# Optimization experiments

Measured on AMD Instinct MI355X. Metric: run time of the kernel, lower is better.

The kernel has to match this reference:

```python
import jax, jax.numpy as jnp
import numpy as np

THRESHOLD = 0.5
NEG_POS_RATIO = 3
ALPHA = 1.0


def xywh2xyxy(b):
    return jnp.concatenate([b[:, :2], b[:, :2] + b[:, 2:]], axis=1)


def cxcy2xyxy(b):
    return jnp.concatenate([b[:, :2] - b[:, 2:] / 2, b[:, :2] + b[:, 2:] / 2], axis=1)


def xyxy2cxcy(b):
    return jnp.concatenate([(b[:, :2] + b[:, 2:]) / 2, b[:, 2:] - b[:, :2]], axis=1)


def jaccard(a, b):
    # a: [n,4], b: [m,4] in xyxy -> IoU [n,m]
    lt = jnp.maximum(a[:, None, :2], b[None, :, :2])
    rb = jnp.minimum(a[:, None, 2:], b[None, :, 2:])
    wh = jnp.clip(rb - lt, 0.0)
    inter = wh[..., 0] * wh[..., 1]
    area_a = (a[:, 2] - a[:, 0]) * (a[:, 3] - a[:, 1])
    area_b = (b[:, 2] - b[:, 0]) * (b[:, 3] - b[:, 1])
    return inter / (area_a[:, None] + area_b[None, :] - inter)


def encode(cxcy, priors_cxcy):
    # cxcy_to_gcxgcy: offsets scaled by /10 variance, log sizes scaled by *5
    return jnp.concatenate([
        (cxcy[:, :2] - priors_cxcy[:, :2]) / (priors_cxcy[:, 2:] / 10.0),
        jnp.log(jnp.abs(cxcy[:, 2:] / priors_cxcy[:, 2:])) * 5.0,
    ], axis=1)


def _match_one(boxes_xywh, labels_i, priors_xy, priors_cxcy):
    n_obj = boxes_xywh.shape[0]
    b_xyxy = xywh2xyxy(boxes_xywh)                      # [n_obj,4]
    ov = jaccard(b_xyxy, priors_xy)                     # [n_obj, P]
    ovl_p = ov.max(axis=0)                              # [P]
    obj_p = ov.argmax(axis=0)                           # [P]
    prior_for_obj = ov.argmax(axis=1)                   # [n_obj]
    # force each object to own its best prior
    obj_p = obj_p.at[prior_for_obj].set(jnp.arange(n_obj))
    ovl_p = ovl_p.at[prior_for_obj].set(1.0)
    lab = labels_i[obj_p]                               # [P]
    lab = jnp.where(ovl_p < THRESHOLD, 0, lab)
    ignore = (ovl_p > 0.4) & (ovl_p < 0.5)
    true_locs = encode(xyxy2cxcy(b_xyxy[obj_p]), priors_cxcy)  # [P,4]
    return lab, ignore, true_locs


def _smooth_l1(x):
    ax = jnp.abs(x)
    return jnp.where(ax < 1.0, 0.5 * ax * ax, ax - 0.5)


def multibox_loss(predicted_locs, predicted_scores, boxes, labels, priors_cxcy):
    priors_xy = cxcy2xyxy(priors_cxcy)
    true_classes, ignored, true_locs = jax.vmap(
        _match_one, in_axes=(0, 0, None, None))(boxes, labels, priors_xy, priors_cxcy)
    pos = (true_classes > 0) & (~ignored)               # [B,P]
    n_pos = pos.sum(axis=1)                             # [B]
    n_pos_total = n_pos.sum()

    # localization loss: SmoothL1 mean over positive-prior elements
    loc_elem = _smooth_l1(predicted_locs - true_locs)   # [B,P,4]
    loc_loss = (loc_elem * pos[..., None]).sum() / (n_pos_total.astype(jnp.float32) * 4.0)

    # per-prior cross entropy
    logp = jax.nn.log_softmax(predicted_scores, axis=-1)           # [B,P,C]
    ce = -jnp.take_along_axis(logp, true_classes[..., None], axis=-1)[..., 0]  # [B,P]

    conf_pos_sum = (ce * pos).sum()
    ce_neg = jnp.where(pos | ignored, 0.0, ce)
    ce_neg_sorted = -jnp.sort(-ce_neg, axis=1)          # descending per row
    ranks = jnp.arange(ce.shape[1])[None, :]
    hard = ranks < (NEG_POS_RATIO * n_pos)[:, None]
    conf_loss = (jnp.where(hard, ce_neg_sorted, 0.0).sum() + conf_pos_sum) / n_pos_total.astype(jnp.float32)

    total = conf_loss + ALPHA * loc_loss
    return total, conf_loss, loc_loss


def setup_inputs() -> dict:
    key = jax.random.key(0)
    k1, k2, k3, k4, k5, k6 = jax.random.split(key, 6)
    B, P, C, NOBJ = 64, 8732, 91, 16
    predicted_locs = jax.random.normal(k1, (B, P, 4), dtype=jnp.float32)
    predicted_scores = jax.random.normal(k2, (B, P, C), dtype=jnp.float32)
    xy = jax.random.uniform(k3, (B, NOBJ, 2)) * 0.6
    wh = jax.random.uniform(k4, (B, NOBJ, 2)) * 0.35 + 0.05
    boxes = jnp.concatenate([xy, wh], axis=-1).astype(jnp.float32)  # xywh
    labels = jax.random.randint(k5, (B, NOBJ), 1, C)
    pxy = jax.random.uniform(k6, (P, 2))
    pwh = jax.random.uniform(jax.random.fold_in(k6, 1), (P, 2)) * 0.45 + 0.05
    priors_cxcy = jnp.concatenate([pxy, pwh], axis=-1).astype(jnp.float32)
    return {"predicted_locs": predicted_locs, "predicted_scores": predicted_scores,
            "boxes": boxes, "labels": labels, "priors_cxcy": priors_cxcy}


def reference(predicted_locs, predicted_scores, boxes, labels, priors_cxcy):
    return multibox_loss(predicted_locs, predicted_scores, boxes, labels, priors_cxcy)
```

## Files before the change

### kernel.cpp

```cpp
#include <hip/hip_runtime.h>
#include <math.h>

#define TPB 256
#define MTPB 512
#define CE_BLOCKS 2048
#define SEGS 4

__device__ __forceinline__ float sl1(float x) {
    float a = fabsf(x);
    return a < 1.f ? 0.5f * a * a : a - 0.5f;
}

template<int NOBJ>
__global__ __launch_bounds__(MTPB)
void k_match_iou(const float* __restrict__ boxes, const float* __restrict__ priors,
                 int P, float* __restrict__ ovl_g, unsigned char* __restrict__ obj_g,
                 float* __restrict__ segv, int* __restrict__ segp,
                 unsigned* __restrict__ ticket)
{
    const int bs = blockIdx.x;
    const int b = bs >> 2;
    const int s = bs & 3;
    const int tid = threadIdx.x;
    const int NW = MTPB / 64;

    if (bs == 0 && tid == 0) *ticket = 0u;

    __shared__ float redv[NOBJ * (MTPB / 64)];
    __shared__ int   redp[NOBJ * (MTPB / 64)];

    const int seglen = (P + SEGS - 1) / SEGS;
    const int p0 = s * seglen;
    const int p1 = min(p0 + seglen, P);

    float bx1[NOBJ], by1[NOBJ], bx2[NOBJ], by2[NOBJ], bar[NOBJ];
#pragma unroll
    for (int o = 0; o < NOBJ; o++) {
        const float4 bx = ((const float4*)boxes)[(size_t)b * NOBJ + o];
        bx1[o] = bx.x; by1[o] = bx.y;
        bx2[o] = bx.x + bx.z; by2[o] = bx.y + bx.w;
        bar[o] = (bx2[o] - bx1[o]) * (by2[o] - by1[o]);
    }

    float bestv[NOBJ];
    int bestp[NOBJ];
#pragma unroll
    for (int o = 0; o < NOBJ; o++) { bestv[o] = -1.f; bestp[o] = 0x7fffffff; }

    for (int p = p0 + tid; p < p1; p += MTPB) {
        float4 pr = ((const float4*)priors)[p];
        float hx = pr.z * 0.5f, hy = pr.w * 0.5f;
        float px1 = pr.x - hx, py1 = pr.y - hy;
        float px2 = pr.x + hx, py2 = pr.y + hy;
        float parea = (px2 - px1) * (py2 - py1);
        float bv = -1.f; int bo = 0;
#pragma unroll
        for (int o = 0; o < NOBJ; o++) {
            float ltx = fmaxf(bx1[o], px1);
            float lty = fmaxf(by1[o], py1);
            float rbx = fminf(bx2[o], px2);
            float rby = fminf(by2[o], py2);
            float w = rbx - ltx; w = w > 0.f ? w : 0.f;
            float h = rby - lty; h = h > 0.f ? h : 0.f;
            float inter = w * h;
            float iou = __fdividef(inter, bar[o] + parea - inter);
            if (iou > bv) { bv = iou; bo = o; }
            if (iou > bestv[o]) { bestv[o] = iou; bestp[o] = p; }
        }
        ovl_g[(size_t)b * P + p] = bv;
        obj_g[(size_t)b * P + p] = (unsigned char)bo;
    }

#pragma unroll
    for (int o = 0; o < NOBJ; o++) {
        float v = bestv[o]; int pp = bestp[o];
#pragma unroll
        for (int d = 1; d < 64; d <<= 1) {
            float v2 = __shfl_xor(v, d);
            int   q2 = __shfl_xor(pp, d);
            if (v2 > v || (v2 == v && q2 < pp)) { v = v2; pp = q2; }
        }
        if ((tid & 63) == 0) {
            redv[o * NW + (tid >> 6)] = v;
            redp[o * NW + (tid >> 6)] = pp;
        }
    }
    __syncthreads();

    if (tid < NOBJ) {
        float v = -2.f; int pp = 0x7fffffff;
        for (int w = 0; w < NW; w++) {
            float v2 = redv[tid * NW + w];
            int   q2 = redp[tid * NW + w];
            if (v2 > v || (v2 == v && q2 < pp)) { v = v2; pp = q2; }
        }
        segv[((size_t)b * NOBJ + tid) * SEGS + s] = v;
        segp[((size_t)b * NOBJ + tid) * SEGS + s] = pp;
    }
}

template<int NOBJ>
__global__ __launch_bounds__(MTPB)
void k_match_fin(const float* __restrict__ boxes, const int* __restrict__ labels,
                 const float* __restrict__ priors, const float* __restrict__ plocs,
                 const float* __restrict__ ovl_g, const unsigned char* __restrict__ obj_g,
                 const float* __restrict__ segv, const int* __restrict__ segp,
                 int P, unsigned* __restrict__ meta,
                 int* __restrict__ n_pos_seg, float* __restrict__ loc_seg)
{
    const int bs = blockIdx.x;
    const int b = bs >> 2;
    const int s = bs & 3;
    const int tid = threadIdx.x;

    __shared__ float sbox2[4 * NOBJ];
    __shared__ int s_lab[NOBJ];
    __shared__ int pf[NOBJ];
    __shared__ int s_cnt;
    __shared__ float s_lsum;

    if (tid < NOBJ) {
        const float4 bx = ((const float4*)boxes)[(size_t)b * NOBJ + tid];
        float x1 = bx.x, y1 = bx.y, x2 = bx.x + bx.z, y2 = bx.y + bx.w;
        sbox2[0 * NOBJ + tid] = (x1 + x2) * 0.5f;
        sbox2[1 * NOBJ + tid] = (y1 + y2) * 0.5f;
        sbox2[2 * NOBJ + tid] = x2 - x1;
        sbox2[3 * NOBJ + tid] = y2 - y1;
        s_lab[tid] = labels[b * NOBJ + tid];
        float v = -2.f; int pp = 0x7fffffff;
#pragma unroll
        for (int ss = 0; ss < SEGS; ss++) {
            float v2 = segv[((size_t)b * NOBJ + tid) * SEGS + ss];
            int   q2 = segp[((size_t)b * NOBJ + tid) * SEGS + ss];
            if (v2 > v || (v2 == v && q2 < pp)) { v = v2; pp = q2; }
        }
        pf[tid] = pp;
        if (tid == 0) { s_cnt = 0; s_lsum = 0.f; }
    }
    __syncthreads();

    const int seglen = (P + SEGS - 1) / SEGS;
    const int p0 = s * seglen;
    const int p1 = min(p0 + seglen, P);

    int cnt = 0;
    float lsum = 0.f;
    for (int p = p0 + tid; p < p1; p += MTPB) {
        float ovl = ovl_g[(size_t)b * P + p];
        int o = obj_g[(size_t)b * P + p];
        int fo = -1;
#pragma unroll
        for (int i = 0; i < NOBJ; i++) if (pf[i] == p) fo = i;
        if (fo >= 0) { ovl = 1.0f; o = fo; }

        int lab = s_lab[o];
        if (ovl < 0.5f) lab = 0;
        bool ign = (ovl > 0.4f) && (ovl < 0.5f);
        bool pos = (lab > 0) && !ign;
        meta[(size_t)b * P + p] = (unsigned)lab | (pos ? 256u : 0u) | (ign ? 512u : 0u);
        if (pos) {
            cnt++;
            float4 pr = ((const float4*)priors)[p];
            float cx = sbox2[0 * NOBJ + o], cy = sbox2[1 * NOBJ + o];
            float bw = sbox2[2 * NOBJ + o], bh = sbox2[3 * NOBJ + o];
            float g0 = (cx - pr.x) / (pr.z / 10.0f);
            float g1 = (cy - pr.y) / (pr.w / 10.0f);
            float g2 = __logf(fabsf(bw / pr.z)) * 5.0f;
            float g3 = __logf(fabsf(bh / pr.w)) * 5.0f;
            float4 pl = ((const float4*)plocs)[(size_t)b * P + p];
            lsum += sl1(pl.x - g0) + sl1(pl.y - g1) + sl1(pl.z - g2) + sl1(pl.w - g3);
        }
    }
#pragma unroll
    for (int d = 1; d < 64; d <<= 1) {
        lsum += __shfl_xor(lsum, d);
        cnt  += __shfl_xor(cnt, d);
    }
    if ((tid & 63) == 0) {
        atomicAdd(&s_cnt, cnt);
        atomicAdd(&s_lsum, lsum);
    }
    __syncthreads();
    if (tid == 0) {
        n_pos_seg[bs] = s_cnt;
        loc_seg[bs] = s_lsum;
    }
}

__global__ __launch_bounds__(TPB)
void k_ce91(const float* __restrict__ scores, const unsigned* __restrict__ meta,
            int BP, float* __restrict__ ce_neg, float* __restrict__ pos_blk)
{
    __shared__ __align__(16) float sf[4 * 364];
    __shared__ float sp[4];

    const int tid = threadIdx.x;
    const int wid = tid >> 6;
    const int lane = tid & 63;
    const int g = (tid >> 4) & 3;
    const int l = tid & 15;
    float* wlds = sf + wid * 364;

    const int nquads = BP >> 2;
    const int gwaves = gridDim.x * (TPB / 64);
    const float4* src = (const float4*)scores;

    float psum = 0.f;

    for (int q = blockIdx.x * (TPB / 64) + wid; q < nquads; q += gwaves) {
        float4 ra = src[(size_t)q * 91 + lane];
        float4 rb = make_float4(0.f, 0.f, 0.f, 0.f);
        if (lane < 27) rb = src[(size_t)q * 91 + 64 + lane];
        unsigned mt = 0u;
        if (l == 0) mt = meta[(q << 2) + g];

        ((float4*)wlds)[lane] = ra;
        if (lane < 27) ((float4*)wlds)[64 + lane] = rb;

        const float* rowp = wlds + g * 91;
        float v[6];
        float m = -INFINITY;
#pragma unroll
        for (int j = 0; j < 6; j++) {
            int idx = l + (j << 4);
            v[j] = (idx < 91) ? rowp[idx] : -INFINITY;
            m = fmaxf(m, v[j]);
        }
#pragma unroll
        for (int d = 1; d < 16; d <<= 1) m = fmaxf(m, __shfl_xor(m, d));

        float se = 0.f;
#pragma unroll
        for (int j = 0; j < 6; j++) se += __expf(v[j] - m);
#pragma unroll
        for (int d = 1; d < 16; d <<= 1) se += __shfl_xor(se, d);

        if (l == 0) {
            int lab = (int)(mt & 255u);
            float sv = rowp[lab];
            float ce = __logf(se) + m - sv;
            bool pos = (mt >> 8) & 1u;
            bool ign = (mt >> 9) & 1u;
            ce_neg[(q << 2) + g] = (pos || ign) ? 0.f : ce;
            if (pos) psum += ce;
        }
    }

#pragma unroll
    for (int d = 1; d < 64; d <<= 1) psum += __shfl_xor(psum, d);
    if ((tid & 63) == 0) sp[tid >> 6] = psum;
    __syncthreads();
    if (tid == 0) pos_blk[blockIdx.x] = sp[0] + sp[1] + sp[2] + sp[3];
}

__global__ __launch_bounds__(TPB)
void k_ce(const float* __restrict__ scores, const unsigned* __restrict__ meta,
          int BP, int C, float* __restrict__ ce_neg, float* __restrict__ pos_blk)
{
    const int tid = threadIdx.x;
    const int g = tid >> 4;
    const int wg = (tid >> 4) & 3;
    const int l = tid & 15;
    const int tiles = BP >> 4;

    float psum = 0.f;

    for (int t = blockIdx.x; t < tiles; t += gridDim.x) {
        const int row = (t << 4) + g;
        const unsigned mt = meta[row];
        const float* s = scores + (size_t)row * C;

        float v[6];
        float m = -INFINITY;
#pragma unroll
        for (int j = 0; j < 6; j++) {
            int idx = l + (j << 4);
            v[j] = (idx < C) ? s[idx] : -INFINITY;
            m = fmaxf(m, v[j]);
        }
#pragma unroll
        for (int d = 1; d < 16; d <<= 1) m = fmaxf(m, __shfl_xor(m, d));

        float se = 0.f;
#pragma unroll
        for (int j = 0; j < 6; j++) se += __expf(v[j] - m);
#pragma unroll
        for (int d = 1; d < 16; d <<= 1) se += __shfl_xor(se, d);

        const int lab = (int)(mt & 255u);
        float pick = v[0];
#pragma unroll
        for (int j = 1; j < 6; j++) pick = ((lab >> 4) == j) ? v[j] : pick;
        float sv = __shfl(pick, (wg << 4) | (lab & 15));

        if (l == 0) {
            float ce = __logf(se) + m - sv;
            bool pos = (mt >> 8) & 1u;
            bool ign = (mt >> 9) & 1u;
            ce_neg[row] = (pos || ign) ? 0.f : ce;
            if (pos) psum += ce;
        }
    }

#pragma unroll
    for (int d = 1; d < 64; d <<= 1) psum += __shfl_xor(psum, d);
    __shared__ float sp[4];
    if ((tid & 63) == 0) sp[tid >> 6] = psum;
    __syncthreads();
    if (tid == 0) pos_blk[blockIdx.x] = sp[0] + sp[1] + sp[2] + sp[3];
}

template<int ITEMS>
__global__ __launch_bounds__(MTPB)
void k_topk_final(const float* __restrict__ ce_neg, const int* __restrict__ n_pos_seg,
                  const float* __restrict__ loc_seg, const float* __restrict__ pos_blk,
                  int nposblk, int P, int B,
                  float* __restrict__ hard, unsigned* __restrict__ ticket,
                  float* __restrict__ out)
{
    const int b = blockIdx.x;
    const int tid = threadIdx.x;
    const float* row = ce_neg + (size_t)b * P;
    __shared__ unsigned cnt[256];
    __shared__ float sm[256];
    __shared__ float s_sumhigh;
    __shared__ unsigned s_pref;
    __shared__ int s_krem;
    __shared__ bool s_last;

    int k = 0;
#pragma unroll
    for (int s = 0; s < SEGS; s++) k += n_pos_seg[b * SEGS + s];
    k *= 3;
    if (k > P) k = P;

    float vals[ITEMS];
#pragma unroll
    for (int i = 0; i < ITEMS; i++) {
        int p = tid + i * MTPB;
        vals[i] = (p < P) ? row[p] : 0.f;
    }

    float hard_b = 0.f;
    if (k > 0) {
        if (tid == 0) { s_sumhigh = 0.f; s_pref = 0u; s_krem = k; }

        for (int shift = 24; shift >= 0; shift -= 8) {
            if (tid < 256) { cnt[tid] = 0u; sm[tid] = 0.f; }
            __syncthreads();

            if (shift == 24) {
#pragma unroll
                for (int i = 0; i < ITEMS; i++) {
                    int p = tid + i * MTPB;
                    float vv = vals[i];
                    unsigned bin = __float_as_uint(vv) >> 24;
                    bool done = (p >= P);
                    while (__any(!done)) {
                        unsigned long long act = __ballot(!done);
                        int leader = (int)__ffsll(act) - 1;
                        unsigned lb = (unsigned)__shfl((int)bin, leader);
                        bool mine = (!done) && (bin == lb);
                        float contrib = mine ? vv : 0.f;
#pragma unroll
                        for (int d = 1; d < 64; d <<= 1)
                            contrib += __shfl_xor(contrib, d);
                        unsigned long long grp = __ballot(mine);
                        if ((tid & 63) == leader) {
                            atomicAdd(&cnt[lb], (unsigned)__popcll(grp));
                            atomicAdd(&sm[lb], contrib);
                        }
                        done = done || mine;
                    }
                }
            } else {
                unsigned pref = s_pref;
                const int high = shift + 8;
#pragma unroll
                for (int i = 0; i < ITEMS; i++) {
                    int p = tid + i * MTPB;
                    float vv = vals[i];
                    unsigned u = __float_as_uint(vv);
                    if (p < P && ((u >> high) == (pref >> high))) {
                        unsigned bin = (u >> shift) & 255u;
                        atomicAdd(&cnt[bin], 1u);
                        atomicAdd(&sm[bin], vv);
                    }
                }
            }
            __syncthreads();
            if (tid == 0) {
                int krem = s_krem;
                float sh = s_sumhigh;
                unsigned p2 = s_pref;
                for (int bin = 255; bin >= 0; --bin) {
                    if ((int)cnt[bin] < krem) { krem -= (int)cnt[bin]; sh += sm[bin]; }
                    else { p2 |= ((unsigned)bin) << shift; break; }
                }
                s_krem = krem; s_sumhigh = sh; s_pref = p2;
            }
            __syncthreads();
        }
        if (tid == 0) {
            float t = __uint_as_float(s_pref);
            hard_b = s_sumhigh + (float)s_krem * t;
        }
    }

    if (tid == 0) {
        atomicExch(&hard[b], hard_b);
        __threadfence();
        unsigned old = atomicAdd(ticket, 1u);
        s_last = (old == (unsigned)(gridDim.x - 1));
    }
    __syncthreads();
    if (!s_last) return;

    __threadfence();
    float hd = (tid < B) ? atomicAdd(&hard[tid], 0.f) : 0.f;
    float lc = 0.f; int np = 0;
    for (int i = tid; i < B * SEGS; i += MTPB) {
        lc += loc_seg[i];
        np += n_pos_seg[i];
    }
    float ps = 0.f;
    for (int i = tid; i < nposblk; i += MTPB) ps += pos_blk[i];

#pragma unroll
    for (int d = 1; d < 64; d <<= 1) {
        hd += __shfl_xor(hd, d);
        lc += __shfl_xor(lc, d);
        ps += __shfl_xor(ps, d);
        np += __shfl_xor(np, d);
    }
    if ((tid & 63) == 0) {
        int wv = tid >> 6;
        sm[wv] = hd; sm[8 + wv] = lc; sm[16 + wv] = ps;
        cnt[wv] = (unsigned)np;
    }
    __syncthreads();
    if (tid == 0) {
        float thd = 0.f, tlc = 0.f, tps = 0.f; unsigned tnp = 0u;
        for (int wv = 0; wv < MTPB / 64; wv++) {
            thd += sm[wv]; tlc += sm[8 + wv]; tps += sm[16 + wv]; tnp += cnt[wv];
        }
        float n = (float)tnp;
        float conf = (thd + tps) / n;
        float loc = tlc / (n * 4.0f);
        out[0] = conf + loc;
        out[1] = conf;
        out[2] = loc;
    }
}

extern "C" void kernel_launch(void* const* d_in, const int* in_sizes, int n_in,
                              void* d_out, int out_size, void* d_ws, size_t ws_size,
                              hipStream_t stream)
{
    const float* plocs  = (const float*)d_in[0];
    const float* scores = (const float*)d_in[1];
    const float* boxes  = (const float*)d_in[2];
    const int*   labels = (const int*)d_in[3];
    const float* priors = (const float*)d_in[4];

    const int P = in_sizes[4] / 4;
    const int B = in_sizes[0] / (P * 4);
    const int C = in_sizes[1] / (B * P);
    const int BP = B * P;
    const int NOBJ = 16;

    char* ws = (char*)d_ws;
    float*    loc_seg   = (float*)ws;
    int*      n_pos_seg = (int*)(ws + 1024);
    float*    hard      = (float*)(ws + 2048);
    unsigned* ticket    = (unsigned*)(ws + 3072);
    unsigned* meta      = (unsigned*)(ws + 4096);
    float*    ce_neg    = (float*)(ws + 4096 + (size_t)BP * 4);
    float*    pos_blk   = (float*)(ws + 4096 + (size_t)BP * 8);
    char*     ws2       = ws + 4096 + (size_t)BP * 8 + 8192;
    float*    segv      = (float*)ws2;
    int*      segp      = (int*)(ws2 + 16384);
    float*    ovl_g     = (float*)(ws2 + 32768);
    unsigned char* obj_g = (unsigned char*)(ws2 + 32768 + (size_t)BP * 4);

    k_match_iou<16><<<B * SEGS, MTPB, 0, stream>>>(boxes, priors, P,
                                                   ovl_g, obj_g, segv, segp, ticket);

    k_match_fin<16><<<B * SEGS, MTPB, 0, stream>>>(boxes, labels, priors, plocs,
                                                   ovl_g, obj_g, segv, segp,
                                                   P, meta, n_pos_seg, loc_seg);

    if (C == 91 && (BP & 3) == 0) {
        k_ce91<<<CE_BLOCKS, TPB, 0, stream>>>(scores, meta, BP, ce_neg, pos_blk);
    } else {
        k_ce<<<CE_BLOCKS, TPB, 0, stream>>>(scores, meta, BP, C, ce_neg, pos_blk);
    }

    if (P <= MTPB * 18) {
        k_topk_final<18><<<B, MTPB, 0, stream>>>(ce_neg, n_pos_seg, loc_seg, pos_blk,
                                                 CE_BLOCKS, P, B, hard, ticket,
                                                 (float*)d_out);
    } else {
        k_topk_final<36><<<B, MTPB, 0, stream>>>(ce_neg, n_pos_seg, loc_seg, pos_blk,
                                                 CE_BLOCKS, P, B, hard, ticket,
                                                 (float*)d_out);
    }
}
```

Before: 133.2 us.

## Pack match threshold flags into byte and double-buffer CE score loads

The IoU match kernel now writes a single byte per prior holding the object index plus two threshold flags (below 0.5, above 0.4), instead of a float overlap and a separate byte. This removes the float overlap round trip through global memory between the match kernels. Separately, the 91-class cross-entropy loop prefetches the next quad's scores and metadata into registers while computing on the current one from a double-buffered LDS slot, overlapping load latency with compute. This adds register and LDS pressure, and the packing relies on NOBJ fitting in 4 bits.

```diff
diff --git a/kernel.cpp b/kernel.cpp
--- a/kernel.cpp
+++ b/kernel.cpp
@@ -14,7 +14,7 @@
 template<int NOBJ>
 __global__ __launch_bounds__(MTPB)
 void k_match_iou(const float* __restrict__ boxes, const float* __restrict__ priors,
-                 int P, float* __restrict__ ovl_g, unsigned char* __restrict__ obj_g,
+                 int P, unsigned char* __restrict__ obj_pack,
                  float* __restrict__ segv, int* __restrict__ segp,
                  unsigned* __restrict__ ticket)
 {
@@ -67,8 +67,10 @@
             if (iou > bv) { bv = iou; bo = o; }
             if (iou > bestv[o]) { bestv[o] = iou; bestp[o] = p; }
         }
-        ovl_g[(size_t)b * P + p] = bv;
-        obj_g[(size_t)b * P + p] = (unsigned char)bo;
+        unsigned char pk = (unsigned char)bo
+                         | (bv < 0.5f ? 0x10 : 0)
+                         | (bv > 0.4f ? 0x20 : 0);
+        obj_pack[(size_t)b * P + p] = pk;
     }
 
 #pragma unroll
@@ -103,7 +105,7 @@
 __global__ __launch_bounds__(MTPB)
 void k_match_fin(const float* __restrict__ boxes, const int* __restrict__ labels,
                  const float* __restrict__ priors, const float* __restrict__ plocs,
-                 const float* __restrict__ ovl_g, const unsigned char* __restrict__ obj_g,
+                 const unsigned char* __restrict__ obj_pack,
                  const float* __restrict__ segv, const int* __restrict__ segp,
                  int P, unsigned* __restrict__ meta,
                  int* __restrict__ n_pos_seg, float* __restrict__ loc_seg)
@@ -146,16 +148,17 @@
     int cnt = 0;
     float lsum = 0.f;
     for (int p = p0 + tid; p < p1; p += MTPB) {
-        float ovl = ovl_g[(size_t)b * P + p];
-        int o = obj_g[(size_t)b * P + p];
+        unsigned pk = obj_pack[(size_t)b * P + p];
+        int o = (int)(pk & 15u);
+        bool lt05 = (pk & 0x10u) != 0;
+        bool gt04 = (pk & 0x20u) != 0;
         int fo = -1;
 #pragma unroll
         for (int i = 0; i < NOBJ; i++) if (pf[i] == p) fo = i;
-        if (fo >= 0) { ovl = 1.0f; o = fo; }
-
-        int lab = s_lab[o];
-        if (ovl < 0.5f) lab = 0;
-        bool ign = (ovl > 0.4f) && (ovl < 0.5f);
+        if (fo >= 0) { o = fo; lt05 = false; gt04 = true; }
+
+        int lab = lt05 ? 0 : s_lab[o];
+        bool ign = gt04 && lt05;
         bool pos = (lab > 0) && !ign;
         meta[(size_t)b * P + p] = (unsigned)lab | (pos ? 256u : 0u) | (ign ? 512u : 0u);
         if (pos) {
@@ -191,7 +194,7 @@
 void k_ce91(const float* __restrict__ scores, const unsigned* __restrict__ meta,
             int BP, float* __restrict__ ce_neg, float* __restrict__ pos_blk)
 {
-    __shared__ __align__(16) float sf[4 * 364];
+    __shared__ __align__(16) float sf[4][2][364];
     __shared__ float sp[4];
 
     const int tid = threadIdx.x;
@@ -199,25 +202,41 @@
     const int lane = tid & 63;
     const int g = (tid >> 4) & 3;
     const int l = tid & 15;
-    float* wlds = sf + wid * 364;
 
     const int nquads = BP >> 2;
-    const int gwaves = gridDim.x * (TPB / 64);
+    const int gw = gridDim.x * (TPB / 64);
     const float4* src = (const float4*)scores;
 
     float psum = 0.f;
 
-    for (int q = blockIdx.x * (TPB / 64) + wid; q < nquads; q += gwaves) {
-        float4 ra = src[(size_t)q * 91 + lane];
-        float4 rb = make_float4(0.f, 0.f, 0.f, 0.f);
+    int q = blockIdx.x * (TPB / 64) + wid;
+    bool have = q < nquads;
+    float4 ra = make_float4(0.f, 0.f, 0.f, 0.f);
+    float4 rb = make_float4(0.f, 0.f, 0.f, 0.f);
+    unsigned mt = 0u;
+    if (have) {
+        ra = src[(size_t)q * 91 + lane];
         if (lane < 27) rb = src[(size_t)q * 91 + 64 + lane];
-        unsigned mt = 0u;
         if (l == 0) mt = meta[(q << 2) + g];
-
-        ((float4*)wlds)[lane] = ra;
-        if (lane < 27) ((float4*)wlds)[64 + lane] = rb;
-
-        const float* rowp = wlds + g * 91;
+    }
+    int buf = 0;
+
+    while (have) {
+        float* wl = &sf[wid][buf][0];
+        ((float4*)wl)[lane] = ra;
+        if (lane < 27) ((float4*)wl)[64 + lane] = rb;
+        const unsigned mt_cur = mt;
+        const int q_cur = q;
+
+        q += gw;
+        have = q < nquads;
+        if (have) {
+            ra = src[(size_t)q * 91 + lane];
+            if (lane < 27) rb = src[(size_t)q * 91 + 64 + lane];
+            if (l == 0) mt = meta[(q << 2) + g];
+        }
+
+        const float* rowp = wl + g * 91;
         float v[6];
         float m = -INFINITY;
 #pragma unroll
@@ -236,14 +255,15 @@
         for (int d = 1; d < 16; d <<= 1) se += __shfl_xor(se, d);
 
         if (l == 0) {
-            int lab = (int)(mt & 255u);
+            int lab = (int)(mt_cur & 255u);
             float sv = rowp[lab];
             float ce = __logf(se) + m - sv;
-            bool pos = (mt >> 8) & 1u;
-            bool ign = (mt >> 9) & 1u;
-            ce_neg[(q << 2) + g] = (pos || ign) ? 0.f : ce;
+            bool pos = (mt_cur >> 8) & 1u;
+            bool ign = (mt_cur >> 9) & 1u;
+            ce_neg[(q_cur << 2) + g] = (pos || ign) ? 0.f : ce;
             if (pos) psum += ce;
         }
+        buf ^= 1;
     }
 
 #pragma unroll
@@ -467,7 +487,6 @@
     const int B = in_sizes[0] / (P * 4);
     const int C = in_sizes[1] / (B * P);
     const int BP = B * P;
-    const int NOBJ = 16;
 
     char* ws = (char*)d_ws;
     float*    loc_seg   = (float*)ws;
@@ -480,14 +499,13 @@
     char*     ws2       = ws + 4096 + (size_t)BP * 8 + 8192;
     float*    segv      = (float*)ws2;
     int*      segp      = (int*)(ws2 + 16384);
-    float*    ovl_g     = (float*)(ws2 + 32768);
-    unsigned char* obj_g = (unsigned char*)(ws2 + 32768 + (size_t)BP * 4);
+    unsigned char* obj_pack = (unsigned char*)(ws2 + 32768);
 
     k_match_iou<16><<<B * SEGS, MTPB, 0, stream>>>(boxes, priors, P,
-                                                   ovl_g, obj_g, segv, segp, ticket);
+                                                   obj_pack, segv, segp, ticket);
 
     k_match_fin<16><<<B * SEGS, MTPB, 0, stream>>>(boxes, labels, priors, plocs,
-                                                   ovl_g, obj_g, segv, segp,
+                                                   obj_pack, segv, segp,
                                                    P, meta, n_pos_seg, loc_seg);
 
     if (C == 91 && (BP & 3) == 0) {
```

New measurement: 133.8 us. About the same (+0.5%).
